# Kernel optimization log

Measured on AMD Instinct MI355X. Metric: run time of the kernel, lower is better.

Reference implementation:

```python
import jax, jax.numpy as jnp
import numpy as np

B = 32768
H = W = 5          # grid_size
NC = 4             # num_colors
E = 64             # embed_dim
HID = 128          # hidden_dim
OUT = 128          # output_dim
NH = 4             # num_heads
HD = E // NH       # head_dim = 16


def _lin(k, fan_in, fan_out):
    w = jax.random.normal(k, (fan_in, fan_out), jnp.float32) / np.sqrt(fan_in)
    b = jnp.zeros((fan_out,), jnp.float32)
    return w, b


def setup_inputs() -> dict:
    key = jax.random.key(0)
    ks = jax.random.split(key, 16)
    obs = jax.random.randint(ks[0], (B, 3, H, W), 0, NC, dtype=jnp.int32)
    color_embed = jax.random.normal(ks[1], (NC, E), jnp.float32)
    row_embed = jax.random.normal(ks[2], (H, E // 2), jnp.float32)
    col_embed = jax.random.normal(ks[3], (W, E // 2), jnp.float32)
    ip_w1, ip_b1 = _lin(ks[4], 2 * E, HID)
    ip_w2, ip_b2 = _lin(ks[5], HID, E)
    q_w, q_b = _lin(ks[6], E, E)
    k_w, k_b = _lin(ks[7], E, E)
    v_w, v_b = _lin(ks[8], E, E)
    o_w, o_b = _lin(ks[9], E, E)
    op_w1, op_b1 = _lin(ks[10], 2 * E, HID)
    op_w2, op_b2 = _lin(ks[11], HID, E)
    cb_w1, cb_b1 = _lin(ks[12], 3 * E, HID)
    cb_w2, cb_b2 = _lin(ks[13], HID, OUT)
    return dict(obs=obs, color_embed=color_embed, row_embed=row_embed, col_embed=col_embed,
                ip_w1=ip_w1, ip_b1=ip_b1, ip_w2=ip_w2, ip_b2=ip_b2,
                q_w=q_w, q_b=q_b, k_w=k_w, k_b=k_b, v_w=v_w, v_b=v_b, o_w=o_w, o_b=o_b,
                op_w1=op_w1, op_b1=op_b1, op_w2=op_w2, op_b2=op_b2,
                cb_w1=cb_w1, cb_b1=cb_b1, cb_w2=cb_w2, cb_b2=cb_b2)


def _mlp(x, w1, b1, w2, b2):
    return jax.nn.relu(x @ w1 + b1) @ w2 + b2


def reference(obs, color_embed, row_embed, col_embed,
              ip_w1, ip_b1, ip_w2, ip_b2,
              q_w, q_b, k_w, k_b, v_w, v_b, o_w, o_b,
              op_w1, op_b1, op_w2, op_b2,
              cb_w1, cb_b1, cb_w2, cb_b2):
    Bn = obs.shape[0]
    input_grid, output_grid, mask = obs[:, 0], obs[:, 1], obs[:, 2]

    # 2D learned positional embedding: concat(row_emb[i], col_emb[j]) -> [H, W, E]
    pos = jnp.concatenate([
        jnp.broadcast_to(row_embed[:, None, :], (H, W, E // 2)),
        jnp.broadcast_to(col_embed[None, :, :], (H, W, E // 2))], axis=-1)
    pos_b = jnp.broadcast_to(pos, (Bn, H, W, E))

    # input branch: color embed + pos -> MLP -> [B, H*W, E]
    in_feat = jnp.concatenate([color_embed[input_grid], pos_b], axis=-1)
    inp_flat = _mlp(in_feat, ip_w1, ip_b1, ip_w2, ip_b2).reshape(Bn, H * W, E)

    # first nonzero mask position per batch (row-major), zero embedding if none
    mflat = (mask != 0).reshape(Bn, H * W)
    has = jnp.any(mflat, axis=1)
    idx = jnp.argmax(mflat, axis=1)
    r, c = idx // W, idx % W
    cpe = jnp.where(has[:, None],
                    jnp.concatenate([row_embed[r], col_embed[c]], axis=-1),
                    0.0)  # [B, E]

    # single-query cross-attention over the 25 input cells
    q = (cpe @ q_w + q_b).reshape(Bn, NH, HD)
    k = (inp_flat @ k_w + k_b).reshape(Bn, H * W, NH, HD)
    v = (inp_flat @ v_w + v_b).reshape(Bn, H * W, NH, HD)
    attn = jax.nn.softmax(jnp.einsum('bhd,bkhd->bhk', q, k) * (HD ** -0.5), axis=-1)
    attended = jnp.einsum('bhk,bkhd->bhd', attn, v).reshape(Bn, E) @ o_w + o_b

    # output branch: MLP then mean-pool over grid
    out_feat = jnp.concatenate([color_embed[output_grid], pos_b], axis=-1)
    out_ctx = _mlp(out_feat, op_w1, op_b1, op_w2, op_b2).mean(axis=(1, 2))

    combined = jnp.concatenate([attended, out_ctx, cpe], axis=-1)  # [B, 3E]
    return _mlp(combined, cb_w1, cb_b1, cb_w2, cb_b2)  # [B, OUT]
```

## Files before the change

kernel.cpp:

```cpp
#include <hip/hip_runtime.h>
#include <hip/hip_bf16.h>


typedef __attribute__((ext_vector_type(8))) short short8v;
typedef __attribute__((ext_vector_type(4))) float float4v;

static __device__ __forceinline__ short f2bfs(float f) {
  __hip_bfloat16 h = __float2bfloat16(f);
  return *reinterpret_cast<short*>(&h);
}
static __device__ __forceinline__ float bfs2f(short s) {
  return __uint_as_float(((unsigned)(unsigned short)s) << 16);
}
static __device__ __forceinline__ unsigned short f2bf(float f) {
  unsigned int u = __float_as_uint(f);
  unsigned int r = (u + 0x7fffu + ((u >> 16) & 1u)) >> 16;
  return (unsigned short)r;
}
static __device__ __forceinline__ float bf2f(unsigned short s) {
  return __uint_as_float(((unsigned int)s) << 16);
}

__global__ void prep12(const float* __restrict__ color_embed,
                       const float* __restrict__ row_embed,
                       const float* __restrict__ col_embed,
                       const float* __restrict__ ip_w1, const float* __restrict__ ip_b1,
                       const float* __restrict__ ip_w2, const float* __restrict__ ip_b2,
                       const float* __restrict__ op_w1, const float* __restrict__ op_b1,
                       const float* __restrict__ op_w2, const float* __restrict__ op_b2,
                       float* __restrict__ inpval, float* __restrict__ outval) {
  __shared__ float feat[128];
  __shared__ float h1[128];
  const int bid = blockIdx.x;
  const int path = bid / 100;
  const int cij = bid % 100;
  const int c = cij / 25, ij = cij % 25, gi = ij / 5, gj = ij % 5;
  const int t = threadIdx.x;
  if (t < 64)      feat[t] = color_embed[c * 64 + t];
  else if (t < 96) feat[t] = row_embed[gi * 32 + (t - 64)];
  else             feat[t] = col_embed[gj * 32 + (t - 96)];
  __syncthreads();
  const float* w1 = path ? op_w1 : ip_w1;
  const float* b1 = path ? op_b1 : ip_b1;
  float acc = b1[t];
#pragma unroll 8
  for (int d = 0; d < 128; ++d) acc = fmaf(feat[d], w1[d * 128 + t], acc);
  h1[t] = fmaxf(acc, 0.f);
  __syncthreads();
  if (t < 64) {
    const float* w2 = path ? op_w2 : ip_w2;
    const float* b2 = path ? op_b2 : ip_b2;
    float v = b2[t];
#pragma unroll 8
    for (int d = 0; d < 128; ++d) v = fmaf(h1[d], w2[d * 64 + t], v);
    (path ? outval : inpval)[cij * 64 + t] = v;
  }
}

__global__ void prep3(const float* __restrict__ row_embed, const float* __restrict__ col_embed,
                      const float* __restrict__ k_w, const float* __restrict__ k_b,
                      const float* __restrict__ v_w, const float* __restrict__ v_b,
                      const float* __restrict__ q_w, const float* __restrict__ q_b,
                      const float* __restrict__ o_w, const float* __restrict__ o_b,
                      const float* __restrict__ cb_w1, const float* __restrict__ cb_b1,
                      const float* __restrict__ inpval, const float* __restrict__ outval,
                      float* __restrict__ ktab, float* __restrict__ vtab,
                      float* __restrict__ outproj, float* __restrict__ qtab,
                      float* __restrict__ cpeproj, float* __restrict__ wov,
                      float* __restrict__ bias1) {
  const int tid = blockIdx.x * 256 + threadIdx.x;
  if (tid < 6400) {
    const int cij = tid >> 6, e2 = tid & 63;
    const float* x = inpval + cij * 64;
    float a = k_b[e2];
#pragma unroll 8
    for (int e = 0; e < 64; ++e) a = fmaf(x[e], k_w[e * 64 + e2], a);
    ktab[tid] = a;
  } else if (tid < 12800) {
    const int l = tid - 6400;
    const int cij = l >> 6, e2 = l & 63;
    const float* x = inpval + cij * 64;
    float a = v_b[e2];
#pragma unroll 8
    for (int e = 0; e < 64; ++e) a = fmaf(x[e], v_w[e * 64 + e2], a);
    vtab[l] = a;
  } else if (tid < 25600) {
    const int l = tid - 12800;
    const int cij = l >> 7, jj = l & 127;
    const float* x = outval + cij * 64;
    float a = 0.f;
#pragma unroll 8
    for (int e = 0; e < 64; ++e) a = fmaf(x[e], cb_w1[(64 + e) * 128 + jj], a);
    outproj[l] = a * (1.f / 25.f);
  } else if (tid < 27264) {
    const int l = tid - 25600;
    const int p = l >> 6, e2 = l & 63;
    float a = q_b[e2];
    if (p < 25) {
      const int r = p / 5, c = p % 5;
#pragma unroll 8
      for (int e = 0; e < 32; ++e) a = fmaf(row_embed[r * 32 + e], q_w[e * 64 + e2], a);
#pragma unroll 8
      for (int e = 0; e < 32; ++e) a = fmaf(col_embed[c * 32 + e], q_w[(32 + e) * 64 + e2], a);
    }
    qtab[l] = a;
  } else if (tid < 30592) {
    const int l = tid - 27264;
    const int p = l >> 7, jj = l & 127;
    float a = 0.f;
    if (p < 25) {
      const int r = p / 5, c = p % 5;
#pragma unroll 8
      for (int e = 0; e < 32; ++e) a = fmaf(row_embed[r * 32 + e], cb_w1[(128 + e) * 128 + jj], a);
#pragma unroll 8
      for (int e = 0; e < 32; ++e) a = fmaf(col_embed[c * 32 + e], cb_w1[(160 + e) * 128 + jj], a);
    }
    cpeproj[l] = a;
  } else if (tid < 38784) {
    const int l = tid - 30592;
    const int d = l >> 7, jj = l & 127;
    float a = 0.f;
#pragma unroll 8
    for (int e = 0; e < 64; ++e) a = fmaf(o_w[d * 64 + e], cb_w1[e * 128 + jj], a);
    wov[l] = a;
  } else if (tid < 38912) {
    const int jj = tid - 38784;
    float a = cb_b1[jj];
#pragma unroll 8
    for (int e = 0; e < 64; ++e) a = fmaf(o_b[e], cb_w1[e * 128 + jj], a);
    bias1[jj] = a;
  }
}

__global__ void prepC(const float* __restrict__ qtab, const float* __restrict__ ktab,
                      const float* __restrict__ wov, const float* __restrict__ cb_w2,
                      const float* __restrict__ outproj, const float* __restrict__ vtab,
                      const float* __restrict__ cpeproj, const float* __restrict__ bias1,
                      float* __restrict__ stab, unsigned short* __restrict__ wovT,
                      unsigned short* __restrict__ cbw2T,
                      unsigned short* __restrict__ vtabT,
                      unsigned short* __restrict__ outprojBT) {
  const int tid = blockIdx.x * 256 + threadIdx.x;
  if (tid < 10400) {
    const int h = tid & 3;
    const int ij = (tid >> 2) % 25;
    const int ig = ((tid >> 2) / 25) & 3;
    const int cpe = (tid >> 2) / 100;
    const float* qq = qtab + cpe * 64 + h * 16;
    const float* kk = ktab + (ig * 25 + ij) * 64 + h * 16;
    float a = 0.f;
#pragma unroll
    for (int d = 0; d < 16; ++d) a = fmaf(qq[d], kk[d], a);
    stab[tid] = a * 0.25f;
  } else if (tid < 18592) {
    const int i = tid - 10400;
    const int j = i >> 6, d = i & 63;
    wovT[i] = f2bf(wov[d * 128 + j]);
  } else if (tid < 34976) {
    const int i = tid - 18592;
    const int j = i >> 7, k = i & 127;
    cbw2T[i] = f2bf(cb_w2[k * 128 + j]);
  } else if (tid < 43168) {
    const int i = tid - 34976;
    const int h = i >> 11, rest = i & 2047;
    const int d = rest >> 7, kp = rest & 127;
    const int ij = kp >> 2, ig = kp & 3;
    vtabT[i] = (ij < 25) ? f2bf(vtab[(ig * 25 + ij) * 64 + h * 16 + d]) : 0;
  } else if (tid < 59552) {
    const int i = tid - 43168;
    const int col = i >> 7, kp = i & 127;
    unsigned short v = 0;
    if (kp < 100) {
      const int ij = kp >> 2, og = kp & 3;
      v = f2bf(outproj[(og * 25 + ij) * 128 + col]);
    } else if (kp < 126) {
      v = f2bf(cpeproj[(kp - 100) * 128 + col]);
    } else if (kp == 126) {
      v = f2bf(bias1[col]);
    }
    outprojBT[i] = v;
  }
}

__global__ __launch_bounds__(256) void arc_fused(
    const int* __restrict__ obs,
    const float* __restrict__ stab,
    const unsigned short* __restrict__ vtabT,
    const unsigned short* __restrict__ outprojBT,
    const unsigned short* __restrict__ wovT,
    const unsigned short* __restrict__ cbw2T,
    const float* __restrict__ cb_b2,
    float* __restrict__ out) {
  __shared__ __align__(16) short lds_w[4 * 16 * 128];
  __shared__ __align__(16) short lds_og[16 * 128];
  __shared__ __align__(16) short lds_raH[16 * 64];
  __shared__ __align__(16) short lds_hidH[16 * 128];
  __shared__ __align__(16) short lds_hidL[16 * 128];

  const int tid = threadIdx.x;
  const int lane = tid & 63, wv = tid >> 6;
  const int row16 = lane & 15, g4 = lane >> 4;
  const int hh = row16 >> 2, jj = row16 & 3;
  const int b_loc = wv * 4 + g4;
  const int rsw = (row16 & 7) << 4;
  const int bswz = (b_loc & 7) << 4;
  const int bbase = blockIdx.x * 64;

  short8v Bv[4], Bo[2][4], Bw[2][2], Bc[2][4];
#pragma unroll
  for (int ks = 0; ks < 4; ++ks)
    Bv[ks] = *(const short8v*)(vtabT + wv * 2048 + row16 * 128 + ks * 32 + g4 * 8);
#pragma unroll
  for (int t = 0; t < 2; ++t) {
    const int col = wv * 32 + t * 16 + row16;
#pragma unroll
    for (int ks = 0; ks < 4; ++ks) {
      Bo[t][ks] = *(const short8v*)(outprojBT + col * 128 + ks * 32 + g4 * 8);
      Bc[t][ks] = *(const short8v*)(cbw2T + col * 128 + ks * 32 + g4 * 8);
    }
#pragma unroll
    for (int ks = 0; ks < 2; ++ks)
      Bw[t][ks] = *(const short8v*)(wovT + col * 64 + ks * 32 + g4 * 8);
  }
  const float bv0 = cb_b2[wv * 32 + row16];
  const float bv1 = cb_b2[wv * 32 + 16 + row16];

  {
    const int4 z = {0, 0, 0, 0};
    int4* pw = (int4*)lds_w;
#pragma unroll
    for (int i = 0; i < 4; ++i) pw[tid + 256 * i] = z;
  }

  int xs[4], ys[4];
#pragma unroll
  for (int e = 0; e < 4; ++e) {
    const int* ob = obs + (bbase + wv * 4 + e) * 75;
    xs[e] = ob[lane];
    ys[e] = (lane < 11) ? ob[64 + lane] : 0;
  }
  __syncthreads();

  for (int it = 0; it < 4; ++it) {
    const int b0 = bbase + it * 16;

    unsigned iglo = 0, ighi = 0, oglo = 0, oghi = 0;
    int cpe_sel = 0;
#pragma unroll
    for (int e = 0; e < 4; ++e) {
      const unsigned long long blo = __ballot(xs[e] & 1);
      const unsigned long long bhi = __ballot(xs[e] & 2);
      const unsigned long long bnzy = __ballot((lane < 11) && (ys[e] != 0));
      const unsigned e_iglo = (unsigned)(blo & 0x1FFFFFFull);
      const unsigned e_ighi = (unsigned)(bhi & 0x1FFFFFFull);
      const unsigned e_oglo = (unsigned)((blo >> 25) & 0x1FFFFFFull);
      const unsigned e_oghi = (unsigned)((bhi >> 25) & 0x1FFFFFFull);
      const unsigned e_mb = (unsigned)(((blo | bhi) >> 50) | (bnzy << 14));
      const int e_cpe = e_mb ? __builtin_ctz(e_mb) : 25;
      if (g4 == e) { iglo = e_iglo; ighi = e_ighi; oglo = e_oglo; oghi = e_oghi; cpe_sel = e_cpe; }
    }

    float ev[7];
    int ig7[7];
    {
      float sv[7];
      float mx = -1e30f;
      const float* sb = stab + cpe_sel * 400 + hh;
#pragma unroll
      for (int m = 0; m < 7; ++m) {
        const int ij = jj + 4 * m;
        if (ij < 25) {
          const int ig = ((iglo >> ij) & 1) | (((ighi >> ij) & 1) << 1);
          ig7[m] = ig;
          sv[m] = sb[ig * 100 + ij * 4];
          mx = fmaxf(mx, sv[m]);
        }
      }
      mx = fmaxf(mx, __shfl_xor(mx, 1));
      mx = fmaxf(mx, __shfl_xor(mx, 2));
      float sum = 0.f;
#pragma unroll
      for (int m = 0; m < 7; ++m) {
        const int ij = jj + 4 * m;
        if (ij < 25) { ev[m] = __expf(sv[m] - mx); sum += ev[m]; }
      }
      sum += __shfl_xor(sum, 1);
      sum += __shfl_xor(sum, 2);
      const float inv = __builtin_amdgcn_rcpf(sum);
#pragma unroll
      for (int m = 0; m < 7; ++m) ev[m] *= inv;
    }

#pragma unroll
    for (int m = 0; m < 7; ++m) {
      const int ij = jj + 4 * m;
      unsigned u0 = 0, u1 = 0;
      if (ij < 25) {
        const unsigned pbu = (unsigned)(unsigned short)f2bfs(ev[m]);
        const int ig = ig7[m];
        u0 = (ig == 0) ? pbu : ((ig == 1) ? (pbu << 16) : 0u);
        u1 = (ig == 2) ? pbu : ((ig == 3) ? (pbu << 16) : 0u);
      }
      const int off = (hh * 4096 + b_loc * 256 + 8 * ij) ^ bswz;
      *(int2*)((char*)lds_w + off) = make_int2((int)u0, (int)u1);
    }

    {
      unsigned sh[8];
#pragma unroll
      for (int u = 0; u < 8; ++u) {
        const int kp = row16 * 8 + u;
        unsigned v = 0;
        if (kp < 100) {
          const int ijq = kp >> 2;
          const int og = ((oglo >> ijq) & 1) | (((oghi >> ijq) & 1) << 1);
          v = (og == (kp & 3)) ? 0x3F80u : 0u;
        } else if (kp < 126) {
          v = (cpe_sel == kp - 100) ? 0x3F80u : 0u;
        } else if (kp == 126) {
          v = 0x3F80u;
        }
        sh[u] = v;
      }
      int4 pk;
      pk.x = (int)(sh[0] | (sh[1] << 16));
      pk.y = (int)(sh[2] | (sh[3] << 16));
      pk.z = (int)(sh[4] | (sh[5] << 16));
      pk.w = (int)(sh[6] | (sh[7] << 16));
      const int off = (b_loc * 256 + row16 * 16) ^ bswz;
      *(int4*)((char*)lds_og + off) = pk;
    }
    __syncthreads();

    float4v rc = {0.f, 0.f, 0.f, 0.f};
#pragma unroll
    for (int ks = 0; ks < 4; ++ks) {
      const short8v a = *(const short8v*)((char*)lds_w +
          ((wv * 4096 + row16 * 256 + ks * 64 + g4 * 16) ^ rsw));
      rc = __builtin_amdgcn_mfma_f32_16x16x32_bf16(a, Bv[ks], rc, 0, 0, 0);
    }
    float4v acc[2];
    acc[0] = (float4v){0.f, 0.f, 0.f, 0.f};
    acc[1] = (float4v){0.f, 0.f, 0.f, 0.f};
#pragma unroll
    for (int ks = 0; ks < 4; ++ks) {
      const short8v a = *(const short8v*)((char*)lds_og +
          ((row16 * 256 + ks * 64 + g4 * 16) ^ rsw));
      acc[0] = __builtin_amdgcn_mfma_f32_16x16x32_bf16(a, Bo[0][ks], acc[0], 0, 0, 0);
      acc[1] = __builtin_amdgcn_mfma_f32_16x16x32_bf16(a, Bo[1][ks], acc[1], 0, 0, 0);
    }

    if (it < 3) {
#pragma unroll
      for (int e = 0; e < 4; ++e) {
        const int* ob = obs + (bbase + (it + 1) * 16 + wv * 4 + e) * 75;
        xs[e] = ob[lane];
        ys[e] = (lane < 11) ? ob[64 + lane] : 0;
      }
    }

#pragma unroll
    for (int r = 0; r < 4; ++r) {
      const int b = g4 * 4 + r;
      const int off = (b * 128 + (wv * 16 + row16) * 2) ^ ((b & 7) << 4);
      *(short*)((char*)lds_raH + off) = f2bfs(rc[r]);
    }
    __syncthreads();

    const short8v aH0 = *(const short8v*)((char*)lds_raH + ((row16 * 128 + g4 * 16) ^ rsw));
    const short8v aH1 = *(const short8v*)((char*)lds_raH + ((row16 * 128 + 64 + g4 * 16) ^ rsw));
#pragma unroll
    for (int t = 0; t < 2; ++t) {
      acc[t] = __builtin_amdgcn_mfma_f32_16x16x32_bf16(aH0, Bw[t][0], acc[t], 0, 0, 0);
      acc[t] = __builtin_amdgcn_mfma_f32_16x16x32_bf16(aH1, Bw[t][1], acc[t], 0, 0, 0);
    }

#pragma unroll
    for (int t = 0; t < 2; ++t) {
      const int col = wv * 32 + t * 16 + row16;
#pragma unroll
      for (int rr = 0; rr < 4; ++rr) {
        const int row = g4 * 4 + rr;
        const float hv = fmaxf(acc[t][rr], 0.f);
        const short hb = f2bfs(hv);
        const int off = (row * 256 + col * 2) ^ ((row & 7) << 4);
        *(short*)((char*)lds_hidH + off) = hb;
        *(short*)((char*)lds_hidL + off) = f2bfs(hv - bfs2f(hb));
      }
    }
    __syncthreads();

    short8v ahH[4], ahL[4];
#pragma unroll
    for (int ks = 0; ks < 4; ++ks) {
      const int off = (row16 * 256 + ks * 64 + g4 * 16) ^ rsw;
      ahH[ks] = *(const short8v*)((char*)lds_hidH + off);
      ahL[ks] = *(const short8v*)((char*)lds_hidL + off);
    }
#pragma unroll
    for (int t = 0; t < 2; ++t) {
      const int col = wv * 32 + t * 16 + row16;
      float4v c2 = {0.f, 0.f, 0.f, 0.f};
#pragma unroll
      for (int ks = 0; ks < 4; ++ks) {
        c2 = __builtin_amdgcn_mfma_f32_16x16x32_bf16(ahL[ks], Bc[t][ks], c2, 0, 0, 0);
        c2 = __builtin_amdgcn_mfma_f32_16x16x32_bf16(ahH[ks], Bc[t][ks], c2, 0, 0, 0);
      }
      const float bv = t ? bv1 : bv0;
#pragma unroll
      for (int rr = 0; rr < 4; ++rr)
        out[(b0 + g4 * 4 + rr) * 128 + col] = c2[rr] + bv;
    }
  }
}

extern "C" void kernel_launch(void* const* d_in, const int* in_sizes, int n_in,
                              void* d_out, int out_size, void* d_ws, size_t ws_size,
                              hipStream_t stream) {
  const int*   obs         = (const int*)d_in[0];
  const float* color_embed = (const float*)d_in[1];
  const float* row_embed   = (const float*)d_in[2];
  const float* col_embed   = (const float*)d_in[3];
  const float* ip_w1 = (const float*)d_in[4];
  const float* ip_b1 = (const float*)d_in[5];
  const float* ip_w2 = (const float*)d_in[6];
  const float* ip_b2 = (const float*)d_in[7];
  const float* q_w = (const float*)d_in[8];
  const float* q_b = (const float*)d_in[9];
  const float* k_w = (const float*)d_in[10];
  const float* k_b = (const float*)d_in[11];
  const float* v_w = (const float*)d_in[12];
  const float* v_b = (const float*)d_in[13];
  const float* o_w = (const float*)d_in[14];
  const float* o_b = (const float*)d_in[15];
  const float* op_w1 = (const float*)d_in[16];
  const float* op_b1 = (const float*)d_in[17];
  const float* op_w2 = (const float*)d_in[18];
  const float* op_b2 = (const float*)d_in[19];
  const float* cb_w1 = (const float*)d_in[20];
  const float* cb_b1 = (const float*)d_in[21];
  const float* cb_w2 = (const float*)d_in[22];
  const float* cb_b2 = (const float*)d_in[23];

  float* ws = (float*)d_ws;
  float* qtab    = ws;
  float* cpeproj = qtab + 1664;
  float* ktab    = cpeproj + 3328;
  float* vtab    = ktab + 6400;
  float* outproj = vtab + 6400;
  float* wov     = outproj + 12800;
  float* bias1   = wov + 8192;
  float* stab    = bias1 + 128;
  unsigned short* wovT      = (unsigned short*)(ws + 49312);
  unsigned short* cbw2T     = (unsigned short*)(ws + 53408);
  unsigned short* vtabT     = (unsigned short*)(ws + 61600);
  unsigned short* outprojBT = (unsigned short*)(ws + 65696);
  float* inpval  = ws + 73888;
  float* outval  = inpval + 6400;

  prep12<<<200, 128, 0, stream>>>(color_embed, row_embed, col_embed,
                                  ip_w1, ip_b1, ip_w2, ip_b2,
                                  op_w1, op_b1, op_w2, op_b2, inpval, outval);
  prep3<<<152, 256, 0, stream>>>(row_embed, col_embed, k_w, k_b, v_w, v_b,
                                 q_w, q_b, o_w, o_b, cb_w1, cb_b1,
                                 inpval, outval,
                                 ktab, vtab, outproj, qtab, cpeproj, wov, bias1);
  prepC<<<233, 256, 0, stream>>>(qtab, ktab, wov, cb_w2, outproj, vtab,
                                 cpeproj, bias1,
                                 stab, wovT, cbw2T, vtabT, outprojBT);
  arc_fused<<<512, 256, 0, stream>>>(obs, stab, vtabT, outprojBT,
                                     wovT, cbw2T, cb_b2, (float*)d_out);
}
```

Measured before the change: 39.64 us.

## Merge three prep kernels into two and halve per-block batch in main kernel

The three weight-preprocessing kernels are collapsed into two launches. The K/V projection, score table, and bf16 transposes are computed directly in their final layouts, so the fp32 intermediate tables for K, V, outproj and wov are no longer written and reread. The main fused kernel now processes 32 batch rows per block over 1024 blocks instead of 64 rows over 512 blocks, trading weight-fragment reuse per block for more parallelism. The intent is to cut launch count and serial dependency latency in the small prep stages.

```diff
diff --git a/kernel.cpp b/kernel.cpp
--- a/kernel.cpp
+++ b/kernel.cpp
@@ -17,168 +17,149 @@
   unsigned int r = (u + 0x7fffu + ((u >> 16) & 1u)) >> 16;
   return (unsigned short)r;
 }
-static __device__ __forceinline__ float bf2f(unsigned short s) {
-  return __uint_as_float(((unsigned int)s) << 16);
-}
-
-__global__ void prep12(const float* __restrict__ color_embed,
-                       const float* __restrict__ row_embed,
-                       const float* __restrict__ col_embed,
-                       const float* __restrict__ ip_w1, const float* __restrict__ ip_b1,
-                       const float* __restrict__ ip_w2, const float* __restrict__ ip_b2,
-                       const float* __restrict__ op_w1, const float* __restrict__ op_b1,
-                       const float* __restrict__ op_w2, const float* __restrict__ op_b2,
-                       float* __restrict__ inpval, float* __restrict__ outval) {
-  __shared__ float feat[128];
-  __shared__ float h1[128];
-  const int bid = blockIdx.x;
-  const int path = bid / 100;
-  const int cij = bid % 100;
-  const int c = cij / 25, ij = cij % 25, gi = ij / 5, gj = ij % 5;
-  const int t = threadIdx.x;
-  if (t < 64)      feat[t] = color_embed[c * 64 + t];
-  else if (t < 96) feat[t] = row_embed[gi * 32 + (t - 64)];
-  else             feat[t] = col_embed[gj * 32 + (t - 96)];
-  __syncthreads();
-  const float* w1 = path ? op_w1 : ip_w1;
-  const float* b1 = path ? op_b1 : ip_b1;
-  float acc = b1[t];
-#pragma unroll 8
-  for (int d = 0; d < 128; ++d) acc = fmaf(feat[d], w1[d * 128 + t], acc);
-  h1[t] = fmaxf(acc, 0.f);
-  __syncthreads();
-  if (t < 64) {
-    const float* w2 = path ? op_w2 : ip_w2;
-    const float* b2 = path ? op_b2 : ip_b2;
-    float v = b2[t];
-#pragma unroll 8
-    for (int d = 0; d < 128; ++d) v = fmaf(h1[d], w2[d * 64 + t], v);
-    (path ? outval : inpval)[cij * 64 + t] = v;
-  }
-}
-
-__global__ void prep3(const float* __restrict__ row_embed, const float* __restrict__ col_embed,
-                      const float* __restrict__ k_w, const float* __restrict__ k_b,
-                      const float* __restrict__ v_w, const float* __restrict__ v_b,
-                      const float* __restrict__ q_w, const float* __restrict__ q_b,
-                      const float* __restrict__ o_w, const float* __restrict__ o_b,
-                      const float* __restrict__ cb_w1, const float* __restrict__ cb_b1,
-                      const float* __restrict__ inpval, const float* __restrict__ outval,
-                      float* __restrict__ ktab, float* __restrict__ vtab,
-                      float* __restrict__ outproj, float* __restrict__ qtab,
-                      float* __restrict__ cpeproj, float* __restrict__ wov,
-                      float* __restrict__ bias1) {
-  const int tid = blockIdx.x * 256 + threadIdx.x;
-  if (tid < 6400) {
-    const int cij = tid >> 6, e2 = tid & 63;
-    const float* x = inpval + cij * 64;
-    float a = k_b[e2];
-#pragma unroll 8
-    for (int e = 0; e < 64; ++e) a = fmaf(x[e], k_w[e * 64 + e2], a);
-    ktab[tid] = a;
-  } else if (tid < 12800) {
-    const int l = tid - 6400;
-    const int cij = l >> 6, e2 = l & 63;
-    const float* x = inpval + cij * 64;
-    float a = v_b[e2];
-#pragma unroll 8
-    for (int e = 0; e < 64; ++e) a = fmaf(x[e], v_w[e * 64 + e2], a);
-    vtab[l] = a;
-  } else if (tid < 25600) {
-    const int l = tid - 12800;
-    const int cij = l >> 7, jj = l & 127;
-    const float* x = outval + cij * 64;
-    float a = 0.f;
-#pragma unroll 8
-    for (int e = 0; e < 64; ++e) a = fmaf(x[e], cb_w1[(64 + e) * 128 + jj], a);
-    outproj[l] = a * (1.f / 25.f);
-  } else if (tid < 27264) {
-    const int l = tid - 25600;
-    const int p = l >> 6, e2 = l & 63;
-    float a = q_b[e2];
-    if (p < 25) {
-      const int r = p / 5, c = p % 5;
-#pragma unroll 8
-      for (int e = 0; e < 32; ++e) a = fmaf(row_embed[r * 32 + e], q_w[e * 64 + e2], a);
-#pragma unroll 8
-      for (int e = 0; e < 32; ++e) a = fmaf(col_embed[c * 32 + e], q_w[(32 + e) * 64 + e2], a);
-    }
-    qtab[l] = a;
-  } else if (tid < 30592) {
-    const int l = tid - 27264;
-    const int p = l >> 7, jj = l & 127;
-    float a = 0.f;
-    if (p < 25) {
-      const int r = p / 5, c = p % 5;
-#pragma unroll 8
-      for (int e = 0; e < 32; ++e) a = fmaf(row_embed[r * 32 + e], cb_w1[(128 + e) * 128 + jj], a);
-#pragma unroll 8
-      for (int e = 0; e < 32; ++e) a = fmaf(col_embed[c * 32 + e], cb_w1[(160 + e) * 128 + jj], a);
-    }
-    cpeproj[l] = a;
-  } else if (tid < 38784) {
-    const int l = tid - 30592;
-    const int d = l >> 7, jj = l & 127;
-    float a = 0.f;
-#pragma unroll 8
-    for (int e = 0; e < 64; ++e) a = fmaf(o_w[d * 64 + e], cb_w1[e * 128 + jj], a);
-    wov[l] = a;
-  } else if (tid < 38912) {
-    const int jj = tid - 38784;
-    float a = cb_b1[jj];
-#pragma unroll 8
-    for (int e = 0; e < 64; ++e) a = fmaf(o_b[e], cb_w1[e * 128 + jj], a);
-    bias1[jj] = a;
-  }
-}
-
-__global__ void prepC(const float* __restrict__ qtab, const float* __restrict__ ktab,
-                      const float* __restrict__ wov, const float* __restrict__ cb_w2,
-                      const float* __restrict__ outproj, const float* __restrict__ vtab,
-                      const float* __restrict__ cpeproj, const float* __restrict__ bias1,
-                      float* __restrict__ stab, unsigned short* __restrict__ wovT,
-                      unsigned short* __restrict__ cbw2T,
-                      unsigned short* __restrict__ vtabT,
-                      unsigned short* __restrict__ outprojBT) {
-  const int tid = blockIdx.x * 256 + threadIdx.x;
-  if (tid < 10400) {
-    const int h = tid & 3;
-    const int ij = (tid >> 2) % 25;
-    const int ig = ((tid >> 2) / 25) & 3;
-    const int cpe = (tid >> 2) / 100;
-    const float* qq = qtab + cpe * 64 + h * 16;
-    const float* kk = ktab + (ig * 25 + ij) * 64 + h * 16;
-    float a = 0.f;
-#pragma unroll
-    for (int d = 0; d < 16; ++d) a = fmaf(qq[d], kk[d], a);
-    stab[tid] = a * 0.25f;
-  } else if (tid < 18592) {
-    const int i = tid - 10400;
-    const int j = i >> 6, d = i & 63;
-    wovT[i] = f2bf(wov[d * 128 + j]);
-  } else if (tid < 34976) {
-    const int i = tid - 18592;
-    const int j = i >> 7, k = i & 127;
-    cbw2T[i] = f2bf(cb_w2[k * 128 + j]);
-  } else if (tid < 43168) {
-    const int i = tid - 34976;
-    const int h = i >> 11, rest = i & 2047;
-    const int d = rest >> 7, kp = rest & 127;
-    const int ij = kp >> 2, ig = kp & 3;
-    vtabT[i] = (ij < 25) ? f2bf(vtab[(ig * 25 + ij) * 64 + h * 16 + d]) : 0;
-  } else if (tid < 59552) {
-    const int i = tid - 43168;
-    const int col = i >> 7, kp = i & 127;
-    unsigned short v = 0;
-    if (kp < 100) {
-      const int ij = kp >> 2, og = kp & 3;
-      v = f2bf(outproj[(og * 25 + ij) * 128 + col]);
-    } else if (kp < 126) {
-      v = f2bf(cpeproj[(kp - 100) * 128 + col]);
-    } else if (kp == 126) {
-      v = f2bf(bias1[col]);
-    }
-    outprojBT[i] = v;
+
+__global__ __launch_bounds__(128) void prepA(
+    const float* __restrict__ color_embed, const float* __restrict__ row_embed,
+    const float* __restrict__ col_embed,
+    const float* __restrict__ ip_w1, const float* __restrict__ ip_b1,
+    const float* __restrict__ ip_w2, const float* __restrict__ ip_b2,
+    const float* __restrict__ op_w1, const float* __restrict__ op_b1,
+    const float* __restrict__ op_w2, const float* __restrict__ op_b2,
+    const float* __restrict__ q_w, const float* __restrict__ q_b,
+    const float* __restrict__ o_w, const float* __restrict__ o_b,
+    const float* __restrict__ cb_w1, const float* __restrict__ cb_b1,
+    const float* __restrict__ cb_w2,
+    float* __restrict__ inpval, float* __restrict__ outval,
+    float* __restrict__ qtab, float* __restrict__ cpeproj,
+    float* __restrict__ bias1,
+    unsigned short* __restrict__ wovT, unsigned short* __restrict__ cbw2T) {
+  const int bid = blockIdx.x, t = threadIdx.x;
+  if (bid < 200) {
+    __shared__ float feat[128];
+    __shared__ float h1[128];
+    const int path = bid / 100;
+    const int cij = bid % 100;
+    const int c = cij / 25, ij = cij % 25, gi = ij / 5, gj = ij % 5;
+    if (t < 64)      feat[t] = color_embed[c * 64 + t];
+    else if (t < 96) feat[t] = row_embed[gi * 32 + (t - 64)];
+    else             feat[t] = col_embed[gj * 32 + (t - 96)];
+    __syncthreads();
+    const float* w1 = path ? op_w1 : ip_w1;
+    const float* b1 = path ? op_b1 : ip_b1;
+    float acc = b1[t];
+#pragma unroll 8
+    for (int d = 0; d < 128; ++d) acc = fmaf(feat[d], w1[d * 128 + t], acc);
+    h1[t] = fmaxf(acc, 0.f);
+    __syncthreads();
+    if (t < 64) {
+      const float* w2 = path ? op_w2 : ip_w2;
+      const float* b2 = path ? op_b2 : ip_b2;
+      float v = b2[t];
+#pragma unroll 8
+      for (int d = 0; d < 128; ++d) v = fmaf(h1[d], w2[d * 64 + t], v);
+      (path ? outval : inpval)[cij * 64 + t] = v;
+    }
+  } else if (bid == 200) {
+    for (int i = t; i < 1664; i += 128) {
+      const int p = i >> 6, e2 = i & 63;
+      float a = q_b[e2];
+      if (p < 25) {
+        const int r = p / 5, cc = p % 5;
+#pragma unroll 8
+        for (int e = 0; e < 32; ++e) a = fmaf(row_embed[r * 32 + e], q_w[e * 64 + e2], a);
+#pragma unroll 8
+        for (int e = 0; e < 32; ++e) a = fmaf(col_embed[cc * 32 + e], q_w[(32 + e) * 64 + e2], a);
+      }
+      qtab[i] = a;
+    }
+    float a = cb_b1[t];
+#pragma unroll 8
+    for (int e = 0; e < 64; ++e) a = fmaf(o_b[e], cb_w1[e * 128 + t], a);
+    bias1[t] = a;
+  } else if (bid == 201) {
+    for (int i = t; i < 3328; i += 128) {
+      const int p = i >> 7, jj = i & 127;
+      float a = 0.f;
+      if (p < 25) {
+        const int r = p / 5, cc = p % 5;
+#pragma unroll 8
+        for (int e = 0; e < 32; ++e) a = fmaf(row_embed[r * 32 + e], cb_w1[(128 + e) * 128 + jj], a);
+#pragma unroll 8
+        for (int e = 0; e < 32; ++e) a = fmaf(col_embed[cc * 32 + e], cb_w1[(160 + e) * 128 + jj], a);
+      }
+      cpeproj[i] = a;
+    }
+  } else if (bid < 206) {
+    const int base = (bid - 202) * 2048;
+    for (int i = t; i < 2048; i += 128) {
+      const int idx = base + i, col = idx >> 6, d = idx & 63;
+      float a = 0.f;
+#pragma unroll 8
+      for (int e = 0; e < 64; ++e) a = fmaf(o_w[d * 64 + e], cb_w1[e * 128 + col], a);
+      wovT[idx] = f2bf(a);
+    }
+  } else {
+    const int base = (bid - 206) * 4096;
+    for (int i = t; i < 4096; i += 128) {
+      const int idx = base + i, col = idx >> 7, k = idx & 127;
+      cbw2T[idx] = f2bf(cb_w2[k * 128 + col]);
+    }
+  }
+}
+
+__global__ __launch_bounds__(128) void prepM(
+    const float* __restrict__ k_w, const float* __restrict__ k_b,
+    const float* __restrict__ v_w, const float* __restrict__ v_b,
+    const float* __restrict__ cb_w1,
+    const float* __restrict__ qtab, const float* __restrict__ cpeproj,
+    const float* __restrict__ bias1,
+    const float* __restrict__ inpval, const float* __restrict__ outval,
+    float* __restrict__ stab, unsigned short* __restrict__ vtabT,
+    unsigned short* __restrict__ outprojBT) {
+  const int bid = blockIdx.x, t = threadIdx.x;
+  if (bid < 100) {
+    __shared__ float kk[64];
+    const int ig = bid / 25, ij = bid % 25;
+    const float* x = inpval + bid * 64;
+    if (t < 64) {
+      float a = k_b[t];
+#pragma unroll 8
+      for (int e = 0; e < 64; ++e) a = fmaf(x[e], k_w[e * 64 + t], a);
+      kk[t] = a;
+    } else {
+      const int e2 = t - 64;
+      float a = v_b[e2];
+#pragma unroll 8
+      for (int e = 0; e < 64; ++e) a = fmaf(x[e], v_w[e * 64 + e2], a);
+      vtabT[(e2 >> 4) * 2048 + (e2 & 15) * 128 + 4 * ij + ig] = f2bf(a);
+    }
+    __syncthreads();
+    {
+      const float* y = outval + bid * 64;
+      float a = 0.f;
+#pragma unroll 8
+      for (int e = 0; e < 64; ++e) a = fmaf(y[e], cb_w1[(64 + e) * 128 + t], a);
+      outprojBT[t * 128 + 4 * ij + ig] = f2bf(a * (1.f / 25.f));
+    }
+    if (t < 104) {
+      const int cpe = t >> 2, h = t & 3;
+      const float* qq = qtab + cpe * 64 + h * 16;
+      float a = 0.f;
+#pragma unroll
+      for (int d = 0; d < 16; ++d) a = fmaf(qq[d], kk[h * 16 + d], a);
+      stab[cpe * 400 + ig * 100 + ij * 4 + h] = a * 0.25f;
+    }
+  } else if (bid == 100) {
+    for (int p = 0; p < 26; ++p)
+      outprojBT[t * 128 + 100 + p] = f2bf(cpeproj[p * 128 + t]);
+    outprojBT[t * 128 + 126] = f2bf(bias1[t]);
+    outprojBT[t * 128 + 127] = 0;
+  } else {
+    for (int i = t; i < 1792; i += 128) {
+      const int h = i / 448, r = i % 448;
+      const int d = r / 28, kp = 100 + r % 28;
+      vtabT[h * 2048 + d * 128 + kp] = 0;
+    }
   }
 }
 
@@ -204,7 +185,7 @@
   const int b_loc = wv * 4 + g4;
   const int rsw = (row16 & 7) << 4;
   const int bswz = (b_loc & 7) << 4;
-  const int bbase = blockIdx.x * 64;
+  const int bbase = blockIdx.x * 32;
 
   short8v Bv[4], Bo[2][4], Bw[2][2], Bc[2][4];
 #pragma unroll
@@ -241,7 +222,7 @@
   }
   __syncthreads();
 
-  for (int it = 0; it < 4; ++it) {
+  for (int it = 0; it < 2; ++it) {
     const int b0 = bbase + it * 16;
 
     unsigned iglo = 0, ighi = 0, oglo = 0, oghi = 0;
@@ -350,10 +331,10 @@
       acc[1] = __builtin_amdgcn_mfma_f32_16x16x32_bf16(a, Bo[1][ks], acc[1], 0, 0, 0);
     }
 
-    if (it < 3) {
+    if (it < 1) {
 #pragma unroll
       for (int e = 0; e < 4; ++e) {
-        const int* ob = obs + (bbase + (it + 1) * 16 + wv * 4 + e) * 75;
+        const int* ob = obs + (bbase + 16 + wv * 4 + e) * 75;
         xs[e] = ob[lane];
         ys[e] = (lane < 11) ? ob[64 + lane] : 0;
       }
@@ -445,29 +426,24 @@
   float* ws = (float*)d_ws;
   float* qtab    = ws;
   float* cpeproj = qtab + 1664;
-  float* ktab    = cpeproj + 3328;
-  float* vtab    = ktab + 6400;
-  float* outproj = vtab + 6400;
-  float* wov     = outproj + 12800;
-  float* bias1   = wov + 8192;
+  float* bias1   = cpeproj + 3328;
   float* stab    = bias1 + 128;
-  unsigned short* wovT      = (unsigned short*)(ws + 49312);
-  unsigned short* cbw2T     = (unsigned short*)(ws + 53408);
-  unsigned short* vtabT     = (unsigned short*)(ws + 61600);
-  unsigned short* outprojBT = (unsigned short*)(ws + 65696);
-  float* inpval  = ws + 73888;
+  unsigned short* wovT      = (unsigned short*)(ws + 15520);
+  unsigned short* cbw2T     = (unsigned short*)(ws + 19616);
+  unsigned short* vtabT     = (unsigned short*)(ws + 27808);
+  unsigned short* outprojBT = (unsigned short*)(ws + 31904);
+  float* inpval  = ws + 40096;
   float* outval  = inpval + 6400;
 
-  prep12<<<200, 128, 0, stream>>>(color_embed, row_embed, col_embed,
-                                  ip_w1, ip_b1, ip_w2, ip_b2,
-                                  op_w1, op_b1, op_w2, op_b2, inpval, outval);
-  prep3<<<152, 256, 0, stream>>>(row_embed, col_embed, k_w, k_b, v_w, v_b,
-                                 q_w, q_b, o_w, o_b, cb_w1, cb_b1,
-                                 inpval, outval,
-                                 ktab, vtab, outproj, qtab, cpeproj, wov, bias1);
-  prepC<<<233, 256, 0, stream>>>(qtab, ktab, wov, cb_w2, outproj, vtab,
-                                 cpeproj, bias1,
-                                 stab, wovT, cbw2T, vtabT, outprojBT);
-  arc_fused<<<512, 256, 0, stream>>>(obs, stab, vtabT, outprojBT,
-                                     wovT, cbw2T, cb_b2, (float*)d_out);
-}
+  prepA<<<210, 128, 0, stream>>>(color_embed, row_embed, col_embed,
+                                 ip_w1, ip_b1, ip_w2, ip_b2,
+                                 op_w1, op_b1, op_w2, op_b2,
+                                 q_w, q_b, o_w, o_b, cb_w1, cb_b1, cb_w2,
+                                 inpval, outval, qtab, cpeproj, bias1,
+                                 wovT, cbw2T);
+  prepM<<<102, 128, 0, stream>>>(k_w, k_b, v_w, v_b, cb_w1,
+                                 qtab, cpeproj, bias1, inpval, outval,
+                                 stab, vtabT, outprojBT);
+  arc_fused<<<1024, 256, 0, stream>>>(obs, stab, vtabT, outprojBT,
+                                      wovT, cbw2T, cb_b2, (float*)d_out);
+}
```

New measurement: 68.01 us. 1.72x slower.

## Software-pipeline obs decode and softmax one iteration ahead of MFMA work

Applied to the files above, without the earlier changes.

Restructures the per-iteration loop so the next tile's obs decode, score lookup and softmax run during the current iteration, after the MFMA issue, and obs loads are prefetched two iterations ahead. The intent is to hide global-load and softmax latency behind matrix work. Input-group indices are packed into one register to limit register growth, though the deeper prefetch may still raise register pressure.

```diff
diff --git a/kernel.cpp b/kernel.cpp
--- a/kernel.cpp
+++ b/kernel.cpp
@@ -16,9 +16,6 @@
   unsigned int u = __float_as_uint(f);
   unsigned int r = (u + 0x7fffu + ((u >> 16) & 1u)) >> 16;
   return (unsigned short)r;
-}
-static __device__ __forceinline__ float bf2f(unsigned short s) {
-  return __uint_as_float(((unsigned int)s) << 16);
 }
 
 __global__ void prep12(const float* __restrict__ color_embed,
@@ -233,19 +230,22 @@
   }
 
   int xs[4], ys[4];
-#pragma unroll
-  for (int e = 0; e < 4; ++e) {
-    const int* ob = obs + (bbase + wv * 4 + e) * 75;
-    xs[e] = ob[lane];
-    ys[e] = (lane < 11) ? ob[64 + lane] : 0;
-  }
-  __syncthreads();
-
-  for (int it = 0; it < 4; ++it) {
-    const int b0 = bbase + it * 16;
-
-    unsigned iglo = 0, ighi = 0, oglo = 0, oghi = 0;
-    int cpe_sel = 0;
+  float ev[7];
+  unsigned igp = 0, oglo = 0, oghi = 0;
+  int cpe_sel = 0;
+
+  auto load_obs = [&](int t) {
+#pragma unroll
+    for (int e = 0; e < 4; ++e) {
+      const int* ob = obs + (bbase + t * 16 + wv * 4 + e) * 75;
+      xs[e] = ob[lane];
+      ys[e] = (lane < 11) ? ob[64 + lane] : 0;
+    }
+  };
+
+  auto decode_softmax = [&]() {
+    unsigned iglo_ = 0, ighi_ = 0;
+    oglo = 0; oghi = 0; cpe_sel = 0;
 #pragma unroll
     for (int e = 0; e < 4; ++e) {
       const unsigned long long blo = __ballot(xs[e] & 1);
@@ -257,39 +257,44 @@
       const unsigned e_oghi = (unsigned)((bhi >> 25) & 0x1FFFFFFull);
       const unsigned e_mb = (unsigned)(((blo | bhi) >> 50) | (bnzy << 14));
       const int e_cpe = e_mb ? __builtin_ctz(e_mb) : 25;
-      if (g4 == e) { iglo = e_iglo; ighi = e_ighi; oglo = e_oglo; oghi = e_oghi; cpe_sel = e_cpe; }
-    }
-
-    float ev[7];
-    int ig7[7];
-    {
-      float sv[7];
-      float mx = -1e30f;
-      const float* sb = stab + cpe_sel * 400 + hh;
-#pragma unroll
-      for (int m = 0; m < 7; ++m) {
-        const int ij = jj + 4 * m;
-        if (ij < 25) {
-          const int ig = ((iglo >> ij) & 1) | (((ighi >> ij) & 1) << 1);
-          ig7[m] = ig;
-          sv[m] = sb[ig * 100 + ij * 4];
-          mx = fmaxf(mx, sv[m]);
-        }
+      if (g4 == e) { iglo_ = e_iglo; ighi_ = e_ighi; oglo = e_oglo; oghi = e_oghi; cpe_sel = e_cpe; }
+    }
+    float sv[7];
+    float mx = -1e30f;
+    igp = 0;
+    const float* sb = stab + cpe_sel * 400 + hh;
+#pragma unroll
+    for (int m = 0; m < 7; ++m) {
+      const int ij = jj + 4 * m;
+      if (ij < 25) {
+        const int ig = ((iglo_ >> ij) & 1) | (((ighi_ >> ij) & 1) << 1);
+        igp |= (unsigned)ig << (2 * m);
+        sv[m] = sb[ig * 100 + ij * 4];
+        mx = fmaxf(mx, sv[m]);
       }
-      mx = fmaxf(mx, __shfl_xor(mx, 1));
-      mx = fmaxf(mx, __shfl_xor(mx, 2));
-      float sum = 0.f;
-#pragma unroll
-      for (int m = 0; m < 7; ++m) {
-        const int ij = jj + 4 * m;
-        if (ij < 25) { ev[m] = __expf(sv[m] - mx); sum += ev[m]; }
-      }
-      sum += __shfl_xor(sum, 1);
-      sum += __shfl_xor(sum, 2);
-      const float inv = __builtin_amdgcn_rcpf(sum);
-#pragma unroll
-      for (int m = 0; m < 7; ++m) ev[m] *= inv;
-    }
+    }
+    mx = fmaxf(mx, __shfl_xor(mx, 1));
+    mx = fmaxf(mx, __shfl_xor(mx, 2));
+    float sum = 0.f;
+#pragma unroll
+    for (int m = 0; m < 7; ++m) {
+      const int ij = jj + 4 * m;
+      if (ij < 25) { ev[m] = __expf(sv[m] - mx); sum += ev[m]; }
+    }
+    sum += __shfl_xor(sum, 1);
+    sum += __shfl_xor(sum, 2);
+    const float inv = __builtin_amdgcn_rcpf(sum);
+#pragma unroll
+    for (int m = 0; m < 7; ++m) ev[m] *= inv;
+  };
+
+  load_obs(0);
+  __syncthreads();
+  decode_softmax();
+  load_obs(1);
+
+  for (int it = 0; it < 4; ++it) {
+    const int b0 = bbase + it * 16;
 
 #pragma unroll
     for (int m = 0; m < 7; ++m) {
@@ -297,7 +302,7 @@
       unsigned u0 = 0, u1 = 0;
       if (ij < 25) {
         const unsigned pbu = (unsigned)(unsigned short)f2bfs(ev[m]);
-        const int ig = ig7[m];
+        const int ig = (int)((igp >> (2 * m)) & 3u);
         u0 = (ig == 0) ? pbu : ((ig == 1) ? (pbu << 16) : 0u);
         u1 = (ig == 2) ? pbu : ((ig == 3) ? (pbu << 16) : 0u);
       }
@@ -351,12 +356,8 @@
     }
 
     if (it < 3) {
-#pragma unroll
-      for (int e = 0; e < 4; ++e) {
-        const int* ob = obs + (bbase + (it + 1) * 16 + wv * 4 + e) * 75;
-        xs[e] = ob[lane];
-        ys[e] = (lane < 11) ? ob[64 + lane] : 0;
-      }
+      decode_softmax();
+      if (it < 2) load_obs(it + 2);
     }
 
 #pragma unroll
```

Result: no change. 40.29 us (+1.6%).
